# Kernel tuning notes

Measured on AMD Instinct MI355X. Metric: run time of the kernel, lower is better.

## Reference

```python
import jax, jax.numpy as jnp
import numpy as np

B, N, H, L = 4096, 512, 1024, 8


def setup_inputs() -> dict:
    key = jax.random.key(0)
    k1, k2, k3, k4 = jax.random.split(key, 4)
    x = jax.random.normal(k1, (B, N), dtype=jnp.float32)
    beta = jax.random.uniform(k2, (H, L, N), dtype=jnp.float32)  # torch.rand init
    bound = 1.0 / np.sqrt(N)
    W = jax.random.uniform(k3, (H, N), minval=-bound, maxval=bound, dtype=jnp.float32)
    b = jax.random.uniform(k4, (H,), minval=-bound, maxval=bound, dtype=jnp.float32)
    return {"x": x, "beta": beta, "W": W, "b": b}


def reference(x, beta, W, b):
    # Original computes c[h,j,k] = sum_l beta[h,l,j]*beta[h,l,k], then
    # out_fm[b,h] = sum_{j<k} x[b,j]*x[b,k]*c[h,j,k]  (strict upper-tri mask).
    # FM identity: sum_{j<k} x_j x_k <v_j, v_k>
    #            = 0.5 * sum_l [ (sum_j x_j v_{lj})^2 - sum_j x_j^2 v_{lj}^2 ]
    s = jnp.einsum('bn,hln->bhl', x, beta)            # (B, H, L)
    ssq = jnp.einsum('bn,hln->bhl', x * x, beta * beta)  # (B, H, L)
    fm = 0.5 * jnp.sum(s * s - ssq, axis=-1)          # (B, H)
    linear_out = x @ W.T + b                          # (B, H)
    return fm + linear_out
```

## Files before the change

### kernel.cpp

```cpp
#include <hip/hip_runtime.h>
#include <stdint.h>

static constexpr int B_DIM = 4096;
static constexpr int N_DIM = 512;
static constexpr int H_DIM = 1024;
static constexpr int L_DIM = 8;
static constexpr int HL    = H_DIM * L_DIM;
static constexpr int KC    = 2 * N_DIM;

typedef __attribute__((ext_vector_type(8))) short short8;
typedef __attribute__((ext_vector_type(8))) unsigned short u16x8;
typedef __attribute__((ext_vector_type(4))) float f32x4;
typedef __attribute__((ext_vector_type(4))) unsigned int u32x4;

__device__ __forceinline__ uint16_t f2bf(float f) {
  uint32_t u = __float_as_uint(f);
  u += 0x7fffu + ((u >> 16) & 1u);
  return (uint16_t)(u >> 16);
}

__device__ __forceinline__ void stage16(const uint16_t* g, uint16_t* l) {
  __builtin_amdgcn_global_load_lds(
      (const __attribute__((address_space(1))) void*)g,
      (__attribute__((address_space(3))) void*)l, 16, 0, 0);
}

__device__ __forceinline__ short8 sq8(short8 a) {
  u32x4 r;
#pragma unroll
  for (int p = 0; p < 4; ++p) {
    float f0 = __uint_as_float(((uint32_t)(uint16_t)a[2 * p])     << 16);
    float f1 = __uint_as_float(((uint32_t)(uint16_t)a[2 * p + 1]) << 16);
    float s0 = f0 * f0, s1 = f1 * f1;
    uint32_t pk;
    asm("v_cvt_pk_bf16_f32 %0, %1, %2" : "=v"(pk) : "v"(s0), "v"(s1));
    r[p] = pk;
  }
  return __builtin_bit_cast(short8, r);
}

static constexpr int PREP_T0 = HL * N_DIM / 8;
static constexpr int PREP_T1 = B_DIM * N_DIM / 8;
static constexpr int PREP_T2 = H_DIM * N_DIM / 8;

__global__ void prep_kernel(const float* __restrict__ x, const float* __restrict__ beta,
                            const float* __restrict__ W,
                            uint16_t* __restrict__ xonly, uint16_t* __restrict__ betab,
                            uint16_t* __restrict__ combW) {
  int t = blockIdx.x * 256 + threadIdx.x;
  if (t < PREP_T0) {
    const f32x4* src = (const f32x4*)(beta + (size_t)t * 8);
    f32x4 a = src[0], b = src[1];
    u16x8 o;
#pragma unroll
    for (int i = 0; i < 4; ++i) { o[i] = f2bf(a[i]); o[4 + i] = f2bf(b[i]); }
    *(u16x8*)(betab + (size_t)t * 8) = o;
    return;
  }
  t -= PREP_T0;
  if (t < PREP_T1) {
    int bb = t >> 6, n8 = (t & 63) * 8;
    const f32x4* src = (const f32x4*)(x + (size_t)bb * N_DIM + n8);
    f32x4 a = src[0], b = src[1];
    u16x8 lo;
#pragma unroll
    for (int i = 0; i < 4; ++i) { lo[i] = f2bf(a[i]); lo[4 + i] = f2bf(b[i]); }
    *(u16x8*)(xonly + (size_t)bb * N_DIM + n8) = lo;
    return;
  }
  t -= PREP_T1;
  int h = t >> 6, n8 = (t & 63) * 8;
  const f32x4* wsrc = (const f32x4*)(W + (size_t)h * N_DIM + n8);
  f32x4 wa = wsrc[0], wb = wsrc[1];
  u16x8 lo;
#pragma unroll
  for (int i = 0; i < 4; ++i) { lo[i] = f2bf(wa[i]); lo[4 + i] = f2bf(wb[i]); }
  *(u16x8*)(combW + (size_t)h * KC + n8) = lo;
  float s[8] = {};
#pragma unroll
  for (int l = 0; l < L_DIM; ++l) {
    const f32x4* bsrc = (const f32x4*)(beta + ((size_t)h * L_DIM + l) * N_DIM + n8);
    f32x4 a = bsrc[0], b = bsrc[1];
#pragma unroll
    for (int i = 0; i < 4; ++i) { s[i] += a[i] * a[i]; s[4 + i] += b[i] * b[i]; }
  }
  u16x8 hi;
#pragma unroll
  for (int i = 0; i < 8; ++i) hi[i] = f2bf(-0.5f * s[i]);
  *(u16x8*)(combW + (size_t)h * KC + N_DIM + n8) = hi;
}

static constexpr int S_BUF = 9216;
static constexpr int OFF_B = 4096;
static constexpr int OFF_W = 8192;

template<bool ODD>
__device__ __forceinline__ void compute_tile(
    const uint16_t* __restrict__ L,
    const int (&offA)[4], const int (&offB)[4], int offW,
    f32x4 (&acc)[4][4], f32x4 (&lacc)[4])
{
  short8 bf[4];
#pragma unroll
  for (int j = 0; j < 4; ++j) bf[j] = *(const short8*)(L + offB[j]);
  short8 wf = *(const short8*)(L + offW);
  __builtin_amdgcn_s_setprio(1);
#pragma unroll
  for (int i = 0; i < 4; ++i) {
    short8 a = *(const short8*)(L + offA[i]);
#pragma unroll
    for (int j = 0; j < 4; ++j)
      acc[i][j] = __builtin_amdgcn_mfma_f32_16x16x32_bf16(a, bf[j], acc[i][j], 0, 0, 0);
    short8 al;
    if constexpr (ODD) al = sq8(a);
    else               al = a;
    lacc[i] = __builtin_amdgcn_mfma_f32_16x16x32_bf16(al, wf, lacc[i], 0, 0, 0);
  }
  __builtin_amdgcn_s_setprio(0);
}

__global__ __launch_bounds__(256) void fm_kernel(
    const uint16_t* __restrict__ xonly,
    const uint16_t* __restrict__ betab,
    const uint16_t* __restrict__ combW,
    const float* __restrict__ bias,
    float* __restrict__ out)
{
  __shared__ __align__(16) uint16_t lds[2 * S_BUF];

  const int tid  = threadIdx.x;
  const int lane = tid & 63;
  const int wave = tid >> 6;
  const int wm = wave >> 1, wn = wave & 1;
  const int fr = lane & 15, quad = lane >> 4;

  const int bid = blockIdx.x;
  const int cid = (bid & 7) * 256 + (bid >> 3);
  const int bx = cid >> 5, by = cid & 31;
  const int row0 = by * 128, col0 = bx * 128, hcol0 = bx * 16;

  const int s0 = tid, s1 = tid + 256;
  const int m0 = s0 >> 2, c0 = (s0 & 3) ^ ((m0 + (m0 >> 2)) & 3);
  const int m1 = s1 >> 2, c1 = (s1 & 3) ^ ((m1 + (m1 >> 2)) & 3);
  const uint16_t* baseA0 = xonly + (size_t)(row0 + m0) * N_DIM + c0 * 8;
  const uint16_t* baseA1 = xonly + (size_t)(row0 + m1) * N_DIM + c1 * 8;
  const uint16_t* baseB0 = betab + (size_t)(col0 + m0) * N_DIM + c0 * 8;
  const uint16_t* baseB1 = betab + (size_t)(col0 + m1) * N_DIM + c1 * 8;
  const int d0 = s0 * 8;
  const int sW = tid & 127;
  const int mW = sW >> 3, cpW = sW & 7, cW = cpW ^ (mW & 7);
  const uint16_t* baseW = combW + (size_t)(hcol0 + mW) * KC
                        + (cW < 4 ? cW * 8 : N_DIM + (cW - 4) * 8);
  const int dW = OFF_W + sW * 8;

  int offA[4], offB[4], offW_;
#pragma unroll
  for (int i = 0; i < 4; ++i) {
    int m = wm * 64 + i * 16 + fr;
    offA[i] = (m * 4 + (quad ^ ((m + (m >> 2)) & 3))) * 8;
  }
#pragma unroll
  for (int j = 0; j < 4; ++j) {
    int m = wn * 64 + j * 16 + fr;
    offB[j] = OFF_B + (m * 4 + (quad ^ ((m + (m >> 2)) & 3))) * 8;
  }
  offW_ = OFF_W + (fr * 8 + ((wn * 4 + quad) ^ (fr & 7))) * 8;

  f32x4 acc[4][4] = {};
  f32x4 lacc[4]   = {};

  auto STAGE = [&](uint16_t* Lp, int kt) {
    stage16(baseA0 + kt, Lp + d0);
    stage16(baseA1 + kt, Lp + d0 + 2048);
    stage16(baseB0 + kt, Lp + OFF_B + d0);
    stage16(baseB1 + kt, Lp + OFF_B + d0 + 2048);
    stage16(baseW + kt, Lp + dW);
  };

  STAGE(lds, 0);
  __syncthreads();

  for (int t = 0; t < 15; ++t) {
    uint16_t* nxt       = lds + ((t & 1) ^ 1) * S_BUF;
    const uint16_t* cur = lds + (t & 1) * S_BUF;
    STAGE(nxt, (t + 1) * 32);
    if (wn) compute_tile<true >(cur, offA, offB, offW_, acc, lacc);
    else    compute_tile<false>(cur, offA, offB, offW_, acc, lacc);
    __syncthreads();
  }
  {
    const uint16_t* cur = lds + S_BUF;
    if (wn) compute_tile<true >(cur, offA, offB, offW_, acc, lacc);
    else    compute_tile<false>(cur, offA, offB, offW_, acc, lacc);
  }
  __syncthreads();

  float* red = (float*)lds;
  if (!wn) {
#pragma unroll
    for (int i = 0; i < 4; ++i)
#pragma unroll
      for (int r = 0; r < 4; ++r)
        red[(wm * 64 + i * 16 + quad * 4 + r) * 20 + fr] = lacc[i][r];
  }
  __syncthreads();
  if (wn) {
#pragma unroll
    for (int i = 0; i < 4; ++i)
#pragma unroll
      for (int r = 0; r < 4; ++r)
        red[(wm * 64 + i * 16 + quad * 4 + r) * 20 + fr] += lacc[i][r];
  }
  __syncthreads();
#pragma unroll
  for (int i = 0; i < 4; ++i)
#pragma unroll
    for (int j = 0; j < 4; ++j) {
      const int hin = wn * 8 + j * 2 + (fr >> 3);
#pragma unroll
      for (int r = 0; r < 4; ++r) {
        float v = acc[i][j][r];
        v = v * v;
        v += __shfl_xor(v, 1);
        v += __shfl_xor(v, 2);
        v += __shfl_xor(v, 4);
        if ((lane & 7) == 0)
          red[(wm * 64 + i * 16 + quad * 4 + r) * 20 + hin] += 0.5f * v;
      }
    }
  __syncthreads();
  {
    const int row = tid >> 1, hb = (tid & 1) * 8;
    const float* rp = red + row * 20 + hb;
    const float* bp = bias + hcol0 + hb;
    float* op = out + (size_t)(row0 + row) * H_DIM + hcol0 + hb;
    f32x4 v0 = *(const f32x4*)(rp);
    f32x4 v1 = *(const f32x4*)(rp + 4);
    f32x4 b0 = *(const f32x4*)(bp);
    f32x4 b1 = *(const f32x4*)(bp + 4);
    *(f32x4*)(op)     = v0 + b0;
    *(f32x4*)(op + 4) = v1 + b1;
  }
}

extern "C" void kernel_launch(void* const* d_in, const int* in_sizes, int n_in,
                              void* d_out, int out_size, void* d_ws, size_t ws_size,
                              hipStream_t stream) {
  const float* x    = (const float*)d_in[0];
  const float* beta = (const float*)d_in[1];
  const float* W    = (const float*)d_in[2];
  const float* bias = (const float*)d_in[3];
  float* out = (float*)d_out;

  uint16_t* xonly = (uint16_t*)d_ws;
  uint16_t* betab = xonly + (size_t)B_DIM * N_DIM;
  uint16_t* combW = betab + (size_t)HL * N_DIM;

  const int prep_threads = PREP_T0 + PREP_T1 + PREP_T2;
  prep_kernel<<<prep_threads / 256, 256, 0, stream>>>(x, beta, W, xonly, betab, combW);

  fm_kernel<<<2048, 256, 0, stream>>>(xonly, betab, combW, bias, out);
}
```

Before: 172.9 us.

## Use single-buffered 128-wide K tiles instead of double-buffered 32-wide tiles

Replaces the double-buffered 32-wide K pipeline (16 iterations, one barrier each) with a single 72KB LDS buffer holding 128-wide K chunks, processed in 4 iterations of 4 MFMA sub-steps, with a new XOR swizzle over 16 column chunks. This cuts the number of barriers and loop iterations. In exchange, global loads no longer overlap with compute: each chunk is loaded, then waited on, then computed. The larger LDS footprint may also reduce how many blocks fit per CU.

```diff
diff --git a/kernel.cpp b/kernel.cpp
--- a/kernel.cpp
+++ b/kernel.cpp
@@ -90,33 +90,36 @@
   *(u16x8*)(combW + (size_t)h * KC + N_DIM + n8) = hi;
 }
 
-static constexpr int S_BUF = 9216;
-static constexpr int OFF_B = 4096;
-static constexpr int OFF_W = 8192;
+static constexpr int OFF_B = 16384;
+static constexpr int OFF_W = 32768;
+static constexpr int S_TOT = 36864;
 
 template<bool ODD>
-__device__ __forceinline__ void compute_tile(
+__device__ __forceinline__ void compute_step(
     const uint16_t* __restrict__ L,
-    const int (&offA)[4], const int (&offB)[4], int offW,
+    const int (&ma)[4], const int (&mb)[4], const int (&sl)[4], const int (&wo)[4],
     f32x4 (&acc)[4][4], f32x4 (&lacc)[4])
 {
-  short8 bf[4];
-#pragma unroll
-  for (int j = 0; j < 4; ++j) bf[j] = *(const short8*)(L + offB[j]);
-  short8 wf = *(const short8*)(L + offW);
-  __builtin_amdgcn_s_setprio(1);
-#pragma unroll
-  for (int i = 0; i < 4; ++i) {
-    short8 a = *(const short8*)(L + offA[i]);
-#pragma unroll
-    for (int j = 0; j < 4; ++j)
-      acc[i][j] = __builtin_amdgcn_mfma_f32_16x16x32_bf16(a, bf[j], acc[i][j], 0, 0, 0);
-    short8 al;
-    if constexpr (ODD) al = sq8(a);
-    else               al = a;
-    lacc[i] = __builtin_amdgcn_mfma_f32_16x16x32_bf16(al, wf, lacc[i], 0, 0, 0);
-  }
-  __builtin_amdgcn_s_setprio(0);
+#pragma unroll
+  for (int kk = 0; kk < 4; ++kk) {
+    short8 bf[4];
+#pragma unroll
+    for (int j = 0; j < 4; ++j) bf[j] = *(const short8*)(L + mb[j] + sl[kk]);
+    short8 wf = *(const short8*)(L + wo[kk]);
+    __builtin_amdgcn_s_setprio(1);
+#pragma unroll
+    for (int i = 0; i < 4; ++i) {
+      short8 a = *(const short8*)(L + ma[i] + sl[kk]);
+#pragma unroll
+      for (int j = 0; j < 4; ++j)
+        acc[i][j] = __builtin_amdgcn_mfma_f32_16x16x32_bf16(a, bf[j], acc[i][j], 0, 0, 0);
+      short8 al;
+      if constexpr (ODD) al = sq8(a);
+      else               al = a;
+      lacc[i] = __builtin_amdgcn_mfma_f32_16x16x32_bf16(al, wf, lacc[i], 0, 0, 0);
+    }
+    __builtin_amdgcn_s_setprio(0);
+  }
 }
 
 __global__ __launch_bounds__(256) void fm_kernel(
@@ -126,7 +129,7 @@
     const float* __restrict__ bias,
     float* __restrict__ out)
 {
-  __shared__ __align__(16) uint16_t lds[2 * S_BUF];
+  __shared__ __align__(16) uint16_t lds[S_TOT];
 
   const int tid  = threadIdx.x;
   const int lane = tid & 63;
@@ -139,59 +142,46 @@
   const int bx = cid >> 5, by = cid & 31;
   const int row0 = by * 128, col0 = bx * 128, hcol0 = bx * 16;
 
-  const int s0 = tid, s1 = tid + 256;
-  const int m0 = s0 >> 2, c0 = (s0 & 3) ^ ((m0 + (m0 >> 2)) & 3);
-  const int m1 = s1 >> 2, c1 = (s1 & 3) ^ ((m1 + (m1 >> 2)) & 3);
-  const uint16_t* baseA0 = xonly + (size_t)(row0 + m0) * N_DIM + c0 * 8;
-  const uint16_t* baseA1 = xonly + (size_t)(row0 + m1) * N_DIM + c1 * 8;
-  const uint16_t* baseB0 = betab + (size_t)(col0 + m0) * N_DIM + c0 * 8;
-  const uint16_t* baseB1 = betab + (size_t)(col0 + m1) * N_DIM + c1 * 8;
-  const int d0 = s0 * 8;
-  const int sW = tid & 127;
-  const int mW = sW >> 3, cpW = sW & 7, cW = cpW ^ (mW & 7);
-  const uint16_t* baseW = combW + (size_t)(hcol0 + mW) * KC
-                        + (cW < 4 ? cW * 8 : N_DIM + (cW - 4) * 8);
-  const int dW = OFF_W + sW * 8;
-
-  int offA[4], offB[4], offW_;
-#pragma unroll
-  for (int i = 0; i < 4; ++i) {
-    int m = wm * 64 + i * 16 + fr;
-    offA[i] = (m * 4 + (quad ^ ((m + (m >> 2)) & 3))) * 8;
-  }
-#pragma unroll
-  for (int j = 0; j < 4; ++j) {
-    int m = wn * 64 + j * 16 + fr;
-    offB[j] = OFF_B + (m * 4 + (quad ^ ((m + (m >> 2)) & 3))) * 8;
-  }
-  offW_ = OFF_W + (fr * 8 + ((wn * 4 + quad) ^ (fr & 7))) * 8;
+  const int cA = (tid & 15) ^ ((tid >> 4) & 15);
+  const uint16_t* baseA = xonly + (size_t)(row0 + (tid >> 4)) * N_DIM + cA * 8;
+  const uint16_t* baseB = betab + (size_t)(col0 + (tid >> 4)) * N_DIM + cA * 8;
+  const int cW = (tid & 31) ^ ((tid >> 5) & 7);
+  const uint16_t* baseW = combW + (size_t)(hcol0 + (tid >> 5)) * KC
+                        + (cW < 16 ? cW * 8 : N_DIM + (cW - 16) * 8);
+  const int dT = tid * 8;
+
+  int ma[4], mb[4], sl[4], wo[4];
+#pragma unroll
+  for (int i = 0; i < 4; ++i) ma[i] = (wm * 64 + i * 16 + fr) * 128;
+#pragma unroll
+  for (int j = 0; j < 4; ++j) mb[j] = OFF_B + (wn * 64 + j * 16 + fr) * 128;
+#pragma unroll
+  for (int kk = 0; kk < 4; ++kk) {
+    sl[kk] = ((kk * 4 + quad) ^ fr) * 8;
+    wo[kk] = OFF_W + (fr * 32 + ((wn * 16 + kk * 4 + quad) ^ (fr & 7))) * 8;
+  }
 
   f32x4 acc[4][4] = {};
   f32x4 lacc[4]   = {};
 
-  auto STAGE = [&](uint16_t* Lp, int kt) {
-    stage16(baseA0 + kt, Lp + d0);
-    stage16(baseA1 + kt, Lp + d0 + 2048);
-    stage16(baseB0 + kt, Lp + OFF_B + d0);
-    stage16(baseB1 + kt, Lp + OFF_B + d0 + 2048);
-    stage16(baseW + kt, Lp + dW);
+  auto STAGE = [&](int kt) {
+#pragma unroll
+    for (int u = 0; u < 8; ++u) {
+      stage16(baseA + kt + (size_t)u * 16 * N_DIM, lds + dT + u * 2048);
+      stage16(baseB + kt + (size_t)u * 16 * N_DIM, lds + OFF_B + dT + u * 2048);
+    }
+#pragma unroll
+    for (int u = 0; u < 2; ++u)
+      stage16(baseW + kt + (size_t)u * 8 * KC, lds + OFF_W + dT + u * 2048);
   };
 
-  STAGE(lds, 0);
-  __syncthreads();
-
-  for (int t = 0; t < 15; ++t) {
-    uint16_t* nxt       = lds + ((t & 1) ^ 1) * S_BUF;
-    const uint16_t* cur = lds + (t & 1) * S_BUF;
-    STAGE(nxt, (t + 1) * 32);
-    if (wn) compute_tile<true >(cur, offA, offB, offW_, acc, lacc);
-    else    compute_tile<false>(cur, offA, offB, offW_, acc, lacc);
+#pragma unroll 1
+  for (int t = 0; t < 4; ++t) {
+    if (t) __syncthreads();
+    STAGE(t * 128);
     __syncthreads();
-  }
-  {
-    const uint16_t* cur = lds + S_BUF;
-    if (wn) compute_tile<true >(cur, offA, offB, offW_, acc, lacc);
-    else    compute_tile<false>(cur, offA, offB, offW_, acc, lacc);
+    if (wn) compute_step<true >(lds, ma, mb, sl, wo, acc, lacc);
+    else    compute_step<false>(lds, ma, mb, sl, wo, acc, lacc);
   }
   __syncthreads();
 
```

After: 242.1 us. +40.0%, slower.
